# Performance work log

Hardware: AMD Instinct MI355X
Metric: run time of the kernel (lower is better)

Reference implementation:

```python
import jax, jax.numpy as jnp
import numpy as np

N = 50000      # nodes
E = 1600000    # edges (before self loops)
IN = 128       # in_channels
HID = 64       # hidden_channels
HEADS = 2
NEG_SLOPE = 0.2  # PyG GATConv default


def setup_inputs() -> dict:
    key = jax.random.key(0)
    ks = jax.random.split(key, 12)
    s = 0.05
    return {
        "x": jax.random.normal(ks[0], (N, IN), jnp.float32),
        "edge_index": jax.random.randint(ks[1], (2, E), 0, N, dtype=jnp.int32),
        # layer 1: GATConv(IN -> HID, heads=HEADS, concat=True)
        "W1": jax.random.normal(ks[2], (IN, HEADS * HID), jnp.float32) * s,
        "a_src1": jax.random.normal(ks[3], (HEADS, HID), jnp.float32) * s,
        "a_dst1": jax.random.normal(ks[4], (HEADS, HID), jnp.float32) * s,
        "b1": jax.random.normal(ks[5], (HEADS * HID,), jnp.float32) * s,
        # layer 2: GATConv(HEADS*HID -> HID, heads=1, concat=False)
        "W2": jax.random.normal(ks[6], (HEADS * HID, HID), jnp.float32) * s,
        "a_src2": jax.random.normal(ks[7], (1, HID), jnp.float32) * s,
        "a_dst2": jax.random.normal(ks[8], (1, HID), jnp.float32) * s,
        "b2": jax.random.normal(ks[9], (HID,), jnp.float32) * s,
        "lin_w": jax.random.normal(ks[10], (HID, 1), jnp.float32) * s,
        "lin_b": jax.random.normal(ks[11], (1,), jnp.float32) * s,
    }


def gat_layer(x, src, dst, W, a_src, a_dst, b, heads, out_ch, concat, n):
    # linear transform: [n, heads, out_ch]
    h = (x @ W).reshape(n, heads, out_ch)
    # per-node attention logit halves  [n, heads]
    al_src = jnp.sum(h * a_src, axis=-1)
    al_dst = jnp.sum(h * a_dst, axis=-1)
    # per-edge logits (gather) + LeakyReLU  [e, heads]
    e = jax.nn.leaky_relu(al_src[src] + al_dst[dst], negative_slope=NEG_SLOPE)
    # segment softmax over edges grouped by destination node
    m = jax.ops.segment_max(e, dst, num_segments=n)
    ex = jnp.exp(e - m[dst])
    denom = jax.ops.segment_sum(ex, dst, num_segments=n)
    alpha = ex / (denom[dst] + 1e-16)
    # weighted message scatter-add  [n, heads, out_ch]
    out = jax.ops.segment_sum(h[src] * alpha[:, :, None], dst, num_segments=n)
    out = out.reshape(n, heads * out_ch) if concat else out.mean(axis=1)
    return out + b


def reference(x, edge_index, W1, a_src1, a_dst1, b1, W2, a_src2, a_dst2, b2, lin_w, lin_b):
    # PyG GATConv adds self loops by default
    loops = jnp.arange(N, dtype=edge_index.dtype)
    src = jnp.concatenate([edge_index[0], loops])
    dst = jnp.concatenate([edge_index[1], loops])
    h = gat_layer(x, src, dst, W1, a_src1, a_dst1, b1, HEADS, HID, True, N)
    h = jax.nn.elu(h)
    h = gat_layer(h, src, dst, W2, a_src2, a_dst2, b2, 1, HID, False, N)
    return (h @ lin_w + lin_b)[:, 0]  # squeeze(-1) -> [N]
```

## Files before the change

### kernel.cpp

```cpp
#include <hip/hip_runtime.h>
#include <hip/hip_fp16.h>


#define LEAKY(x) ((x) > 0.f ? (x) : 0.2f * (x))

typedef float v2f __attribute__((ext_vector_type(2)));
typedef _Float16 f16x8 __attribute__((ext_vector_type(8)));
typedef __fp16 h16x2 __attribute__((ext_vector_type(2)));
typedef float f32x4 __attribute__((ext_vector_type(4)));


__global__ __launch_bounds__(256) void zero_kernel(int* __restrict__ bcnt,
                                                   int* __restrict__ bcur_rel,
                                                   int* __restrict__ off,
                                                   int B, int n, int Etot) {
  if (threadIdx.x <= (unsigned)B) {
    bcnt[threadIdx.x] = 0;
    bcur_rel[threadIdx.x] = 0;
  }
  if (threadIdx.x == 255) off[n] = Etot;
}


template <int VPT>
__global__ __launch_bounds__(256) void prep_cnt_kernel(const float* __restrict__ W1,
                                                       const float* __restrict__ W2,
                                                       const float* __restrict__ as2,
                                                       const float* __restrict__ ad2,
                                                       const float* __restrict__ lw,
                                                       unsigned short* __restrict__ Wp1,
                                                       float* __restrict__ vsrc2,
                                                       float* __restrict__ vdst2,
                                                       float* __restrict__ vlin,
                                                       const int* __restrict__ ei, int E, int n,
                                                       int* __restrict__ bc, int WB) {
  if ((int)blockIdx.x < WB) {
    int t = blockIdx.x * 256 + threadIdx.x;
    if (t < 16384) {
      int e = t;
      int i = e & 7;
      int c = (e >> 3) & 15;
      int g = (e >> 7) & 3;
      int kk = (e >> 9) & 3;
      int cn = e >> 11;
      int k = kk * 32 + g * 8 + i;
      int col = cn * 16 + c;
      __half h = __float2half(W1[k * 128 + col]);
      Wp1[e] = *(unsigned short*)&h;
    } else if (t < 16384 + 128) {
      int k = t - 16384;
      float a = 0.f, b = 0.f, s = 0.f;
      for (int cc = 0; cc < 64; ++cc) {
        float w = W2[k * 64 + cc];
        a = fmaf(w, as2[cc], a);
        b = fmaf(w, ad2[cc], b);
        s = fmaf(w, lw[cc], s);
      }
      vsrc2[k] = a;
      vdst2[k] = b;
      vlin[k] = s;
    }
    return;
  }
  __shared__ int lc[256];
  int t = threadIdx.x;
  lc[t] = 0;
  __syncthreads();
  int base = (blockIdx.x - WB) * (256 * VPT) + t;
  int tot = E + n;
#pragma unroll
  for (int u = 0; u < VPT; ++u) {
    int i = base + u * 256;
    if (i < tot) {
      int d = (i < E) ? ei[E + i] : (i - E);
      atomicAdd(&lc[d >> 8], 1);
    }
  }
  __syncthreads();
  if (lc[t]) atomicAdd(&bc[t], lc[t]);
}


template <int VPT>
__global__ __launch_bounds__(256) void gemm_scatter_kernel(
    const float* __restrict__ X, const uint4* __restrict__ Wp,
    const float* __restrict__ a_src, const float* __restrict__ a_dst,
    unsigned char* __restrict__ Hout, float2* __restrict__ als, float2* __restrict__ ald,
    const int* __restrict__ ei, int E, int n,
    const int* __restrict__ bcnt, int* __restrict__ bcur_rel,
    unsigned* __restrict__ entries, int B, int GB) {
  if ((int)blockIdx.x < GB) {
    __shared__ float Xl[32 * 132];
    __shared__ float lgt[2][2][2][16];
    int t = threadIdx.x;
    int wave = t >> 6, lane = t & 63;
    int wm = wave >> 1, wn = wave & 1;
    int g = lane >> 4, c = lane & 15;
    int nb0 = blockIdx.x * 32;

    {
      const float4* Xg = (const float4*)X;
      float4* Xs = (float4*)Xl;
#pragma unroll
      for (int u = 0; u < 4; ++u) {
        int idx = u * 256 + t;
        int r = idx >> 5, c4 = idx & 31;
        int row = nb0 + r;
        int rc = row < n ? row : (n - 1);
        Xs[r * 33 + c4] = Xg[(size_t)rc * 32 + c4];
      }
    }
    __syncthreads();

    f16x8 af[4];
    const float* xr = Xl + (wm * 16 + c) * 132 + g * 8;
#pragma unroll
    for (int kk = 0; kk < 4; ++kk) {
      float4 x0 = *(const float4*)(xr + kk * 32);
      float4 x1 = *(const float4*)(xr + kk * 32 + 4);
      union { f16x8 v; h16x2 p[4]; } A;
      A.p[0] = __builtin_amdgcn_cvt_pkrtz(x0.x, x0.y);
      A.p[1] = __builtin_amdgcn_cvt_pkrtz(x0.z, x0.w);
      A.p[2] = __builtin_amdgcn_cvt_pkrtz(x1.x, x1.y);
      A.p[3] = __builtin_amdgcn_cvt_pkrtz(x1.z, x1.w);
      af[kk] = A.v;
    }

    f32x4 acc[4];
    f32x4 z = {0.f, 0.f, 0.f, 0.f};
#pragma unroll
    for (int cn = 0; cn < 4; ++cn) acc[cn] = z;
#pragma unroll
    for (int cn = 0; cn < 4; ++cn) {
      int cng = wn * 4 + cn;
#pragma unroll
      for (int kk = 0; kk < 4; ++kk) {
        union { uint4 u; f16x8 v; } Bf;
        Bf.u = Wp[(cng * 4 + kk) * 64 + lane];
        acc[cn] = __builtin_amdgcn_mfma_f32_16x16x32_f16(af[kk], Bf.v, acc[cn], 0, 0, 0);
      }
    }

    float asv[4], adv[4];
#pragma unroll
    for (int cn = 0; cn < 4; ++cn) {
      int col_l = wn * 64 + cn * 16 + c;
      asv[cn] = a_src[col_l];
      adv[cn] = a_dst[col_l];
    }
    float ps[4] = {0.f, 0.f, 0.f, 0.f};
    float pd[4] = {0.f, 0.f, 0.f, 0.f};
#pragma unroll
    for (int cn = 0; cn < 4; ++cn) {
#pragma unroll
      for (int r = 0; r < 4; ++r) {
        float v = acc[cn][r];
        ps[r] = fmaf(v, asv[cn], ps[r]);
        pd[r] = fmaf(v, adv[cn], pd[r]);
        int noder = nb0 + wm * 16 + g * 4 + r;
        int colg = wn * 64 + cn * 16 + c;
        if (noder < n) {
          int b8 = __builtin_amdgcn_cvt_pk_fp8_f32(v, v, 0, false);
          Hout[(size_t)noder * 128 + colg] = (unsigned char)(b8 & 0xff);
        }
      }
    }
#pragma unroll
    for (int r = 0; r < 4; ++r) {
#pragma unroll
      for (int m = 1; m <= 8; m <<= 1) {
        ps[r] += __shfl_xor(ps[r], m, 64);
        pd[r] += __shfl_xor(pd[r], m, 64);
      }
    }
    if (c == 0) {
#pragma unroll
      for (int r = 0; r < 4; ++r) {
        lgt[wm][wn][0][g * 4 + r] = ps[r];
        lgt[wm][wn][1][g * 4 + r] = pd[r];
      }
    }
    __syncthreads();
    if (t < 32) {
      int wmm = t >> 4, row = t & 15;
      int node = nb0 + wmm * 16 + row;
      if (node < n) {
        als[node] = make_float2(lgt[wmm][0][0][row], lgt[wmm][1][0][row]);
        ald[node] = make_float2(lgt[wmm][0][1][row], lgt[wmm][1][1][row]);
      }
    }
    return;
  }
  __shared__ int lc[256];
  __shared__ int lbase[256];
  __shared__ int bscan[256];
  int t = threadIdx.x;
  lc[t] = 0;
  int v = (t < B) ? bcnt[t] : 0;
  bscan[t] = v;
  __syncthreads();
  for (int s = 1; s < 256; s <<= 1) {
    int a = (t >= s) ? bscan[t - s] : 0;
    __syncthreads();
    bscan[t] += a;
    __syncthreads();
  }
  int excl = bscan[t] - v;

  int base = (blockIdx.x - GB) * (256 * VPT) + t;
  int tot = E + n;
  int bb[VPT], ll[VPT];
  unsigned pk[VPT];
#pragma unroll
  for (int u = 0; u < VPT; ++u) {
    int i = base + u * 256;
    bb[u] = -1;
    if (i < tot) {
      int s, d;
      if (i < E) { s = ei[i]; d = ei[E + i]; }
      else       { s = d = i - E; }
      int b = d >> 8;
      bb[u] = b;
      ll[u] = atomicAdd(&lc[b], 1);
      pk[u] = (unsigned)s | ((unsigned)(d & 255) << 16);
    }
  }
  __syncthreads();
  if (lc[t]) lbase[t] = excl + atomicAdd(&bcur_rel[t], lc[t]);
  __syncthreads();
#pragma unroll
  for (int u = 0; u < VPT; ++u)
    if (bb[u] >= 0) entries[lbase[bb[u]] + ll[u]] = pk[u];
}


__global__ __launch_bounds__(1024) void csr_build_kernel(const unsigned* __restrict__ entries,
                                                         const int* __restrict__ bcnt,
                                                         int* __restrict__ off,
                                                         unsigned short* __restrict__ eps,
                                                         int n, int B) {
  __shared__ int bscan[256];
  __shared__ int hist[256];
  __shared__ int scn[256];
  __shared__ int cur[256];
  int b = blockIdx.x, t = threadIdx.x;
  if (t < 256) bscan[t] = (t < B) ? bcnt[t] : 0;
  __syncthreads();
  for (int s = 1; s < 256; s <<= 1) {
    int a = (t >= (unsigned)s && t < 256) ? bscan[t - s] : 0;
    __syncthreads();
    if (t < 256) bscan[t] += a;
    __syncthreads();
  }
  int k0 = (b == 0) ? 0 : bscan[b - 1];
  int k1 = bscan[b];

  if (t < 256) hist[t] = 0;
  __syncthreads();
  for (int k = k0 + t; k < k1; k += 1024) atomicAdd(&hist[(entries[k] >> 16) & 255], 1);
  __syncthreads();
  int hv = (t < 256) ? hist[t] : 0;
  if (t < 256) scn[t] = hv;
  __syncthreads();
  for (int s = 1; s < 256; s <<= 1) {
    int a = (t >= (unsigned)s && t < 256) ? scn[t - s] : 0;
    __syncthreads();
    if (t < 256) scn[t] += a;
    __syncthreads();
  }
  if (t < 256) {
    int excl = scn[t] - hv;
    int d = (b << 8) + t;
    if (d < n) off[d] = k0 + excl;
    cur[t] = k0 + excl;
  }
  __syncthreads();
  for (int k = k0 + t; k < k1; k += 1024) {
    unsigned e = entries[k];
    unsigned dl = (e >> 16) & 255;
    int p = atomicAdd(&cur[dl], 1);
    eps[p] = (unsigned short)(e & 0xffffu);
  }
}


__global__ __launch_bounds__(256) void agg1_kernel(const unsigned char* __restrict__ Hb8,
                                                   const float2* __restrict__ als,
                                                   const float2* __restrict__ ald,
                                                   const unsigned short* __restrict__ eps,
                                                   const int* __restrict__ off,
                                                   const float* __restrict__ b1,
                                                   const float* __restrict__ vsrc2,
                                                   const float* __restrict__ vdst2,
                                                   const float* __restrict__ vlin,
                                                   float2* __restrict__ gsrc,
                                                   float* __restrict__ adst2, int n) {
  __shared__ float wlds[4][128];
  int wid = (blockIdx.x * 256 + threadIdx.x) >> 6;
  int lane = threadIdx.x & 63;
  if (wid >= n) return;
  wid = __builtin_amdgcn_readfirstlane(wid);
  int wslot = (threadIdx.x >> 6) & 3;
  int sel = lane >> 5;
  int c31 = lane & 31;
  int head = c31 >> 4;
  int k0 = off[wid], k1 = off[wid + 1];
  const unsigned* Hd = (const unsigned*)Hb8;
  float2 advv = ald[wid];
  int wbase = head * 64 + sel;

  float a0 = 0.f, a1 = 0.f, a2 = 0.f, a3 = 0.f, den0 = 0.f, den1 = 0.f;

  for (int kb = k0; kb < k1; kb += 64) {
    int rem = min(k1 - kb, 64);
    int e = kb + (lane < rem ? lane : rem - 1);
    unsigned pp = eps[e];
    float2 l = als[pp];
    float g0 = __expf(LEAKY(l.x + advv.x));
    float g1 = __expf(LEAKY(l.y + advv.y));
    bool ok = lane < rem;
    wlds[wslot][lane] = ok ? g0 : 0.f;
    wlds[wslot][64 + lane] = ok ? g1 : 0.f;
    if (ok) { den0 += g0; den1 += g1; }
    int npair = (rem + 1) >> 1;

#define PAIR1(qq)                                                                   \
  {                                                                                 \
    unsigned p = (unsigned)__shfl((int)pp, ((qq) << 1) + sel, 64);                  \
    float w = wlds[wslot][wbase + ((qq) << 1)];                                     \
    unsigned hv = Hd[p * 32u + (unsigned)c31];                                      \
    v2f lo = __builtin_amdgcn_cvt_pk_f32_fp8((int)hv, false);                       \
    v2f hi = __builtin_amdgcn_cvt_pk_f32_fp8((int)hv, true);                        \
    a0 = fmaf(lo.x, w, a0);                                                         \
    a1 = fmaf(lo.y, w, a1);                                                         \
    a2 = fmaf(hi.x, w, a2);                                                         \
    a3 = fmaf(hi.y, w, a3);                                                         \
  }

    int nb = npair >> 3;
    for (int b = 0; b < nb; ++b) {
      int qb = b << 3;
#pragma unroll
      for (int q = 0; q < 8; ++q) PAIR1(qb + q);
    }
    for (int q = nb << 3; q < npair; ++q) PAIR1(q);
#undef PAIR1
  }

  a0 += __shfl_xor(a0, 32, 64);
  a1 += __shfl_xor(a1, 32, 64);
  a2 += __shfl_xor(a2, 32, 64);
  a3 += __shfl_xor(a3, 32, 64);
#pragma unroll
  for (int m = 1; m <= 32; m <<= 1) {
    den0 += __shfl_xor(den0, m, 64);
    den1 += __shfl_xor(den1, m, 64);
  }
  float den = head ? den1 : den0;

  float inv = 1.f / (den + 1e-16f);
  float4 bv = ((const float4*)b1)[c31];
  float r0 = a0 * inv + bv.x;
  float r1 = a1 * inv + bv.y;
  float r2 = a2 * inv + bv.z;
  float r3 = a3 * inv + bv.w;
  r0 = r0 > 0.f ? r0 : (__expf(r0) - 1.f);
  r1 = r1 > 0.f ? r1 : (__expf(r1) - 1.f);
  r2 = r2 > 0.f ? r2 : (__expf(r2) - 1.f);
  r3 = r3 > 0.f ? r3 : (__expf(r3) - 1.f);
  float4 vs = ((const float4*)vsrc2)[c31];
  float4 vd = ((const float4*)vdst2)[c31];
  float4 vl = ((const float4*)vlin)[c31];
  float ps = r0 * vs.x + r1 * vs.y + r2 * vs.z + r3 * vs.w;
  float pd = r0 * vd.x + r1 * vd.y + r2 * vd.z + r3 * vd.w;
  float sv = r0 * vl.x + r1 * vl.y + r2 * vl.z + r3 * vl.w;
#pragma unroll
  for (int m = 1; m <= 16; m <<= 1) {
    ps += __shfl_xor(ps, m, 64);
    pd += __shfl_xor(pd, m, 64);
    sv += __shfl_xor(sv, m, 64);
  }
  if (lane == 0) {
    gsrc[wid] = make_float2(ps, sv);
    adst2[wid] = pd;
  }
}


__global__ __launch_bounds__(256) void agg2_kernel(const float2* __restrict__ gsrc,
                                                   const float* __restrict__ adst2,
                                                   const unsigned short* __restrict__ eps,
                                                   const int* __restrict__ off,
                                                   const float* __restrict__ b2,
                                                   const float* __restrict__ lin_w,
                                                   const float* __restrict__ lin_b,
                                                   float* __restrict__ out, int n) {
  int wid = (blockIdx.x * 256 + threadIdx.x) >> 6;
  int lane = threadIdx.x & 63;
  if (wid >= n) return;
  wid = __builtin_amdgcn_readfirstlane(wid);
  int k0 = off[wid], k1 = off[wid + 1];
  float adv = adst2[wid];

  float num = 0.f, den = 0.f;
  for (int kb = k0; kb < k1; kb += 64) {
    int e = kb + lane;
    bool ok = e < k1;
    unsigned pp = eps[ok ? e : k0];
    float2 g = gsrc[pp];
    float w = ok ? __expf(LEAKY(g.x + adv)) : 0.f;
    num = fmaf(w, g.y, num);
    den += w;
  }
  float bt = b2[lane] * lin_w[lane];
#pragma unroll
  for (int m = 1; m <= 32; m <<= 1) {
    num += __shfl_xor(num, m, 64);
    den += __shfl_xor(den, m, 64);
    bt  += __shfl_xor(bt, m, 64);
  }
  if (lane == 0) out[wid] = num / (den + 1e-16f) + bt + lin_b[0];
}


static inline size_t alignup(size_t v) { return (v + 255) & ~(size_t)255; }

extern "C" void kernel_launch(void* const* d_in, const int* in_sizes, int n_in,
                              void* d_out, int out_size, void* d_ws, size_t ws_size,
                              hipStream_t stream) {
  const float* x   = (const float*)d_in[0];
  const int*   ei  = (const int*)d_in[1];
  const float* W1  = (const float*)d_in[2];
  const float* as1 = (const float*)d_in[3];
  const float* ad1 = (const float*)d_in[4];
  const float* b1  = (const float*)d_in[5];
  const float* W2  = (const float*)d_in[6];
  const float* as2 = (const float*)d_in[7];
  const float* ad2 = (const float*)d_in[8];
  const float* b2  = (const float*)d_in[9];
  const float* lw  = (const float*)d_in[10];
  const float* lb  = (const float*)d_in[11];
  float* out = (float*)d_out;

  const int N = out_size;
  const int E = in_sizes[1] / 2;
  const int Etot = E + N;
  const int B = (N + 255) >> 8;

  char* p = (char*)d_ws;
  int* bcnt = (int*)p;  p += alignup((size_t)(B + 1) * 4);
  int* bcur_rel = (int*)p; p += alignup((size_t)(B + 1) * 4);
  unsigned* entries = (unsigned*)p; p += alignup((size_t)Etot * 4);
  int* off  = (int*)p;  p += alignup((size_t)(N + 1) * 4);
  unsigned short* eps = (unsigned short*)p; p += alignup((size_t)Etot * 2);
  float2* als = (float2*)p; p += alignup((size_t)N * 8);
  float2* ald = (float2*)p; p += alignup((size_t)N * 8);
  float2* gsrc = (float2*)p; p += alignup((size_t)N * 8);
  float* adst2 = (float*)p; p += alignup((size_t)N * 4);
  unsigned char* h1b = (unsigned char*)p; p += alignup((size_t)N * 128);
  unsigned short* wp1 = (unsigned short*)p; p += alignup((size_t)16384 * 2);
  float* vsrc2 = (float*)p; p += alignup((size_t)128 * 4);
  float* vdst2 = (float*)p; p += alignup((size_t)128 * 4);
  float* vlin  = (float*)p; p += alignup((size_t)128 * 4);

  constexpr int VPT = 8;
  int egrid = (Etot + 256 * VPT - 1) / (256 * VPT);
  constexpr int WB = 65;
  int GB = (N + 31) / 32;

  zero_kernel<<<1, 256, 0, stream>>>(bcnt, bcur_rel, off, B, N, Etot);
  prep_cnt_kernel<VPT><<<WB + egrid, 256, 0, stream>>>(
      W1, W2, as2, ad2, lw, wp1, vsrc2, vdst2, vlin, ei, E, N, bcnt, WB);
  gemm_scatter_kernel<VPT><<<GB + egrid, 256, 0, stream>>>(
      x, (const uint4*)wp1, as1, ad1, h1b, als, ald,
      ei, E, N, bcnt, bcur_rel, entries, B, GB);
  csr_build_kernel<<<B, 1024, 0, stream>>>(entries, bcnt, off, eps, N, B);

  agg1_kernel<<<(N + 3) / 4, 256, 0, stream>>>(h1b, als, ald, eps, off, b1,
                                               vsrc2, vdst2, vlin, gsrc, adst2, N);
  agg2_kernel<<<(N + 3) / 4, 256, 0, stream>>>(gsrc, adst2, eps, off, b2, lw, lb, out, N);
}
```

Before: 127.6 us.

## Split layer-1 features into per-head planes and aggregate each head separately

```diff
diff --git a/kernel.cpp b/kernel.cpp
--- a/kernel.cpp
+++ b/kernel.cpp
@@ -150,6 +150,7 @@
     }
     float ps[4] = {0.f, 0.f, 0.f, 0.f};
     float pd[4] = {0.f, 0.f, 0.f, 0.f};
+    size_t plane0 = (size_t)wn * ((size_t)n * 64);
 #pragma unroll
     for (int cn = 0; cn < 4; ++cn) {
 #pragma unroll
@@ -158,10 +159,10 @@
         ps[r] = fmaf(v, asv[cn], ps[r]);
         pd[r] = fmaf(v, adv[cn], pd[r]);
         int noder = nb0 + wm * 16 + g * 4 + r;
-        int colg = wn * 64 + cn * 16 + c;
+        int colp = cn * 16 + c;
         if (noder < n) {
           int b8 = __builtin_amdgcn_cvt_pk_fp8_f32(v, v, 0, false);
-          Hout[(size_t)noder * 128 + colg] = (unsigned char)(b8 & 0xff);
+          Hout[plane0 + (size_t)noder * 64 + colp] = (unsigned char)(b8 & 0xff);
         }
       }
     }
@@ -284,51 +285,52 @@
 }
 
 
-__global__ __launch_bounds__(256) void agg1_kernel(const unsigned char* __restrict__ Hb8,
-                                                   const float2* __restrict__ als,
-                                                   const float2* __restrict__ ald,
-                                                   const unsigned short* __restrict__ eps,
-                                                   const int* __restrict__ off,
-                                                   const float* __restrict__ b1,
-                                                   const float* __restrict__ vsrc2,
-                                                   const float* __restrict__ vdst2,
-                                                   const float* __restrict__ vlin,
-                                                   float2* __restrict__ gsrc,
-                                                   float* __restrict__ adst2, int n) {
-  __shared__ float wlds[4][128];
+template <int HEAD, int FINAL>
+__global__ __launch_bounds__(256) void agg1_pass_kernel(const unsigned char* __restrict__ Hplane,
+                                                        const float2* __restrict__ als,
+                                                        const float2* __restrict__ ald,
+                                                        const unsigned short* __restrict__ eps,
+                                                        const int* __restrict__ off,
+                                                        const float* __restrict__ b1,
+                                                        const float* __restrict__ vsrc2,
+                                                        const float* __restrict__ vdst2,
+                                                        const float* __restrict__ vlin,
+                                                        float4* __restrict__ part,
+                                                        float2* __restrict__ gsrc,
+                                                        float* __restrict__ adst2, int n) {
+  __shared__ float wlds[4][64];
   int wid = (blockIdx.x * 256 + threadIdx.x) >> 6;
   int lane = threadIdx.x & 63;
   if (wid >= n) return;
   wid = __builtin_amdgcn_readfirstlane(wid);
   int wslot = (threadIdx.x >> 6) & 3;
-  int sel = lane >> 5;
-  int c31 = lane & 31;
-  int head = c31 >> 4;
+  int grp = lane >> 4;
+  int c16 = lane & 15;
   int k0 = off[wid], k1 = off[wid + 1];
-  const unsigned* Hd = (const unsigned*)Hb8;
-  float2 advv = ald[wid];
-  int wbase = head * 64 + sel;
-
-  float a0 = 0.f, a1 = 0.f, a2 = 0.f, a3 = 0.f, den0 = 0.f, den1 = 0.f;
+  const unsigned* Hd = (const unsigned*)Hplane;
+  float2 adt = ald[wid];
+  float adv = HEAD ? adt.y : adt.x;
+
+  float a0 = 0.f, a1 = 0.f, a2 = 0.f, a3 = 0.f, den = 0.f;
 
   for (int kb = k0; kb < k1; kb += 64) {
     int rem = min(k1 - kb, 64);
     int e = kb + (lane < rem ? lane : rem - 1);
     unsigned pp = eps[e];
     float2 l = als[pp];
-    float g0 = __expf(LEAKY(l.x + advv.x));
-    float g1 = __expf(LEAKY(l.y + advv.y));
+    float lg = HEAD ? l.y : l.x;
+    float g = __expf(LEAKY(lg + adv));
     bool ok = lane < rem;
-    wlds[wslot][lane] = ok ? g0 : 0.f;
-    wlds[wslot][64 + lane] = ok ? g1 : 0.f;
-    if (ok) { den0 += g0; den1 += g1; }
-    int npair = (rem + 1) >> 1;
-
-#define PAIR1(qq)                                                                   \
+    wlds[wslot][lane] = ok ? g : 0.f;
+    if (ok) den += g;
+    int nquad = (rem + 3) >> 2;
+
+#define QUAD1(qq)                                                                   \
   {                                                                                 \
-    unsigned p = (unsigned)__shfl((int)pp, ((qq) << 1) + sel, 64);                  \
-    float w = wlds[wslot][wbase + ((qq) << 1)];                                     \
-    unsigned hv = Hd[p * 32u + (unsigned)c31];                                      \
+    int idx = ((qq) << 2) + grp;                                                    \
+    unsigned p = (unsigned)__shfl((int)pp, idx, 64);                                \
+    float w = wlds[wslot][idx];                                                     \
+    unsigned hv = Hd[p * 16u + (unsigned)c16];                                      \
     v2f lo = __builtin_amdgcn_cvt_pk_f32_fp8((int)hv, false);                       \
     v2f hi = __builtin_amdgcn_cvt_pk_f32_fp8((int)hv, true);                        \
     a0 = fmaf(lo.x, w, a0);                                                         \
@@ -337,29 +339,28 @@
     a3 = fmaf(hi.y, w, a3);                                                         \
   }
 
-    int nb = npair >> 3;
+    int nb = nquad >> 3;
     for (int b = 0; b < nb; ++b) {
       int qb = b << 3;
 #pragma unroll
-      for (int q = 0; q < 8; ++q) PAIR1(qb + q);
-    }
-    for (int q = nb << 3; q < npair; ++q) PAIR1(q);
-#undef PAIR1
-  }
-
-  a0 += __shfl_xor(a0, 32, 64);
-  a1 += __shfl_xor(a1, 32, 64);
-  a2 += __shfl_xor(a2, 32, 64);
-  a3 += __shfl_xor(a3, 32, 64);
-#pragma unroll
-  for (int m = 1; m <= 32; m <<= 1) {
-    den0 += __shfl_xor(den0, m, 64);
-    den1 += __shfl_xor(den1, m, 64);
-  }
-  float den = head ? den1 : den0;
+      for (int q = 0; q < 8; ++q) QUAD1(qb + q);
+    }
+    for (int q = nb << 3; q < nquad; ++q) QUAD1(q);
+#undef QUAD1
+  }
+
+#pragma unroll
+  for (int m = 16; m <= 32; m <<= 1) {
+    a0 += __shfl_xor(a0, m, 64);
+    a1 += __shfl_xor(a1, m, 64);
+    a2 += __shfl_xor(a2, m, 64);
+    a3 += __shfl_xor(a3, m, 64);
+  }
+#pragma unroll
+  for (int m = 1; m <= 32; m <<= 1) den += __shfl_xor(den, m, 64);
 
   float inv = 1.f / (den + 1e-16f);
-  float4 bv = ((const float4*)b1)[c31];
+  float4 bv = ((const float4*)(b1 + HEAD * 64))[c16];
   float r0 = a0 * inv + bv.x;
   float r1 = a1 * inv + bv.y;
   float r2 = a2 * inv + bv.z;
@@ -368,21 +369,26 @@
   r1 = r1 > 0.f ? r1 : (__expf(r1) - 1.f);
   r2 = r2 > 0.f ? r2 : (__expf(r2) - 1.f);
   r3 = r3 > 0.f ? r3 : (__expf(r3) - 1.f);
-  float4 vs = ((const float4*)vsrc2)[c31];
-  float4 vd = ((const float4*)vdst2)[c31];
-  float4 vl = ((const float4*)vlin)[c31];
+  float4 vs = ((const float4*)(vsrc2 + HEAD * 64))[c16];
+  float4 vd = ((const float4*)(vdst2 + HEAD * 64))[c16];
+  float4 vl = ((const float4*)(vlin + HEAD * 64))[c16];
   float ps = r0 * vs.x + r1 * vs.y + r2 * vs.z + r3 * vs.w;
   float pd = r0 * vd.x + r1 * vd.y + r2 * vd.z + r3 * vd.w;
   float sv = r0 * vl.x + r1 * vl.y + r2 * vl.z + r3 * vl.w;
 #pragma unroll
-  for (int m = 1; m <= 16; m <<= 1) {
+  for (int m = 1; m <= 8; m <<= 1) {
     ps += __shfl_xor(ps, m, 64);
     pd += __shfl_xor(pd, m, 64);
     sv += __shfl_xor(sv, m, 64);
   }
   if (lane == 0) {
-    gsrc[wid] = make_float2(ps, sv);
-    adst2[wid] = pd;
+    if (FINAL) {
+      float4 pr = part[wid];
+      gsrc[wid] = make_float2(ps + pr.x, sv + pr.z);
+      adst2[wid] = pd + pr.y;
+    } else {
+      part[wid] = make_float4(ps, pd, sv, 0.f);
+    }
   }
 }
 
@@ -457,6 +463,7 @@
   float2* ald = (float2*)p; p += alignup((size_t)N * 8);
   float2* gsrc = (float2*)p; p += alignup((size_t)N * 8);
   float* adst2 = (float*)p; p += alignup((size_t)N * 4);
+  float4* part = (float4*)p; p += alignup((size_t)N * 16);
   unsigned char* h1b = (unsigned char*)p; p += alignup((size_t)N * 128);
   unsigned short* wp1 = (unsigned short*)p; p += alignup((size_t)16384 * 2);
   float* vsrc2 = (float*)p; p += alignup((size_t)128 * 4);
@@ -467,6 +474,7 @@
   int egrid = (Etot + 256 * VPT - 1) / (256 * VPT);
   constexpr int WB = 65;
   int GB = (N + 31) / 32;
+  size_t plane = (size_t)N * 64;
 
   zero_kernel<<<1, 256, 0, stream>>>(bcnt, bcur_rel, off, B, N, Etot);
   prep_cnt_kernel<VPT><<<WB + egrid, 256, 0, stream>>>(
@@ -476,7 +484,9 @@
       ei, E, N, bcnt, bcur_rel, entries, B, GB);
   csr_build_kernel<<<B, 1024, 0, stream>>>(entries, bcnt, off, eps, N, B);
 
-  agg1_kernel<<<(N + 3) / 4, 256, 0, stream>>>(h1b, als, ald, eps, off, b1,
-                                               vsrc2, vdst2, vlin, gsrc, adst2, N);
+  agg1_pass_kernel<0, 0><<<(N + 3) / 4, 256, 0, stream>>>(
+      h1b, als, ald, eps, off, b1, vsrc2, vdst2, vlin, part, gsrc, adst2, N);
+  agg1_pass_kernel<1, 1><<<(N + 3) / 4, 256, 0, stream>>>(
+      h1b + plane, als, ald, eps, off, b1, vsrc2, vdst2, vlin, part, gsrc, adst2, N);
   agg2_kernel<<<(N + 3) / 4, 256, 0, stream>>>(gsrc, adst2, eps, off, b2, lw, lb, out, N);
 }
```

Measured after the change: 144.3 us. 13.0% more time.
